# Performance work log

Measured on AMD Instinct MI355X. Metric: run time of the kernel, lower is better.

Reference implementation:

```python
import jax, jax.numpy as jnp
import numpy as np

EPS = 1e-5


def _layernorm(x, w, b):
    mu = jnp.mean(x, axis=-1, keepdims=True)
    var = jnp.var(x, axis=-1, keepdims=True)
    return (x - mu) * jax.lax.rsqrt(var + EPS) * w + b


def setup_inputs() -> dict:
    key = jax.random.key(0)
    ks = jax.random.split(key, 3)
    h, dff = 1024, 4096
    x = jax.random.normal(ks[0], (4, 2048, h), dtype=jnp.float32)
    w1 = jax.random.normal(ks[1], (h, dff), dtype=jnp.float32) * (1.0 / np.sqrt(h))
    w2 = jax.random.normal(ks[2], (dff, h), dtype=jnp.float32) * (1.0 / np.sqrt(dff))
    return {
        "x": x,
        "ln1_w": jnp.ones((h,), jnp.float32),
        "ln1_b": jnp.zeros((h,), jnp.float32),
        "ln2_w": jnp.ones((h,), jnp.float32),
        "ln2_b": jnp.zeros((h,), jnp.float32),
        "w1": w1,
        "b1": jnp.zeros((dff,), jnp.float32),
        "w2": w2,
        "b2": jnp.zeros((h,), jnp.float32),
    }


def reference(x, ln1_w, ln1_b, ln2_w, ln2_b, w1, b1, w2, b2):
    # double 1D FFT: over hidden (dim=-1) then sequence (dim=-2), keep real part
    fourier_x = jnp.fft.fft(jnp.fft.fft(x, axis=-1), axis=-2).real
    x = x + fourier_x
    x = _layernorm(x, ln1_w, ln1_b)
    # FFN: Linear -> exact GELU -> Linear (dropout is identity in eval)
    h = jax.nn.gelu(jnp.einsum("bsd,df->bsf", x, w1) + b1, approximate=False)
    x = x + jnp.einsum("bsf,fd->bsd", h, w2) + b2
    return _layernorm(x, ln2_w, ln2_b)
```

## Files before the change

### kernel.cpp

```cpp
#include <hip/hip_runtime.h>
#include <hip/hip_bf16.h>
#include <math.h>

typedef __bf16 bf16_t;
typedef __bf16 bf16x8 __attribute__((ext_vector_type(8)));
typedef __bf16 bf16x4 __attribute__((ext_vector_type(4)));
typedef float  f32x4  __attribute__((ext_vector_type(4)));

#define NROWS 8192
#define HD    1024
#define DFF   4096
#define HKEEP 513

typedef __attribute__((address_space(1))) const void* gas_cptr;
typedef __attribute__((address_space(3))) void* las_ptr;

__device__ __forceinline__ void gload_lds16(const void* g, void* l) {
  __builtin_amdgcn_global_load_lds((gas_cptr)g, (las_ptr)l, 16, 0, 0);
}

template <int N> __device__ __forceinline__ void vmw() {
  if      constexpr (N==4)  asm volatile("s_waitcnt vmcnt(4)"  ::: "memory");
  else if constexpr (N==6)  asm volatile("s_waitcnt vmcnt(6)"  ::: "memory");
  else if constexpr (N==7)  asm volatile("s_waitcnt vmcnt(7)"  ::: "memory");
  else if constexpr (N==8)  asm volatile("s_waitcnt vmcnt(8)"  ::: "memory");
  else if constexpr (N==10) asm volatile("s_waitcnt vmcnt(10)" ::: "memory");
}

__global__ __launch_bounds__(256) void transpose_to_bf16(
    const float* __restrict__ in, bf16_t* __restrict__ out, int R, int C)
{
  __shared__ float tile[32][33];
  const int bx = blockIdx.x, by = blockIdx.y;
  const int tx = threadIdx.x, ty = threadIdx.y;
  #pragma unroll
  for (int i = ty; i < 32; i += 8)
    tile[i][tx] = in[(size_t)(by*32 + i)*C + bx*32 + tx];
  __syncthreads();
  #pragma unroll
  for (int i = ty; i < 32; i += 8)
    out[(size_t)(bx*32 + i)*R + by*32 + tx] = (bf16_t)tile[tx][i];
}

#define RPB 16
#define LDW 1036
__global__ __launch_bounds__(512) void fft_h_t(
    const float* __restrict__ x, float* __restrict__ reT, float* __restrict__ imT)
{
  __shared__ float sre[RPB*LDW], sim[RPB*LDW], twc[512], tws[512];
  const int t = threadIdx.x;
  const int row0 = blockIdx.x * RPB;
  {
    float sv, cv; sincosf(-6.28318530717958647692f * (float)t * (1.0f/1024.0f), &sv, &cv);
    twc[t] = cv; tws[t] = sv;
  }
  #pragma unroll
  for (int q = 0; q < 8; ++q) {
    const int i = t + 512*q;
    const int row = i >> 8, c4 = i & 255;
    float4 v = *(const float4*)(x + (size_t)(row0+row)*HD + c4*4);
    *(float4*)&sre[row*LDW + c4*4] = v;
  }
  __syncthreads();
  const int b0i = __brev((unsigned)t) >> 22;
  const int b1i = __brev((unsigned)(t + 512)) >> 22;
  float rv[32];
  #pragma unroll
  for (int q = 0; q < 16; ++q) {
    rv[2*q]   = sre[q*LDW + b0i];
    rv[2*q+1] = sre[q*LDW + b1i];
  }
  __syncthreads();
  #pragma unroll
  for (int q = 0; q < 16; ++q) {
    sre[q*LDW + t]       = rv[2*q];
    sre[q*LDW + t + 512] = rv[2*q+1];
    sim[q*LDW + t]       = 0.0f;
    sim[q*LDW + t + 512] = 0.0f;
  }
  __syncthreads();
  for (int s = 0; s < 10; ++s) {
    const int half = 1 << s;
    const int j    = t & (half - 1);
    const int ib   = ((t >> s) << (s + 1)) | j;
    const int ti2  = j << (9 - s);
    const float wc = twc[ti2], ws = tws[ti2];
    #pragma unroll
    for (int q = 0; q < 16; ++q) {
      float* pr = &sre[q*LDW]; float* pi = &sim[q*LDW];
      const float r1 = pr[ib],      i1v = pi[ib];
      const float r2 = pr[ib+half], i2v = pi[ib+half];
      const float tr = r2*wc - i2v*ws;
      const float ti = r2*ws + i2v*wc;
      pr[ib]      = r1 + tr; pi[ib]      = i1v + ti;
      pr[ib+half] = r1 - tr; pi[ib+half] = i1v - ti;
    }
    __syncthreads();
  }
  const int tx = t & 15, th = t >> 4;
  #pragma unroll
  for (int hh = 0; hh < 17; ++hh) {
    const int h = hh*32 + th;
    if (h < HKEEP) {
      reT[(size_t)h*NROWS + row0 + tx] = sre[tx*LDW + h];
      imT[(size_t)h*NROWS + row0 + tx] = sim[tx*LDW + h];
    }
  }
}

__global__ __launch_bounds__(256) void fft_s_col(
    const float* __restrict__ reT, const float* __restrict__ imT,
    float* __restrict__ fT)
{
  __shared__ float sre[2048], sim[2048], twc[1024], tws[1024];
  const int t = threadIdx.x;
  const int h = blockIdx.x;
  const int batch = blockIdx.y;
  const size_t base = (size_t)h * NROWS + batch * 2048;
  for (int k = t; k < 1024; k += 256) {
    float sv, cv; sincosf(-6.28318530717958647692f * (float)k * (1.0f/2048.0f), &sv, &cv);
    twc[k] = cv; tws[k] = sv;
  }
  #pragma unroll
  for (int q = 0; q < 8; ++q) {
    const int i = t + 256*q;
    const int src = __brev((unsigned)i) >> 21;
    sre[i] = reT[base + src];
    sim[i] = imT[base + src];
  }
  __syncthreads();
  for (int s = 0; s < 11; ++s) {
    const int half = 1 << s;
    #pragma unroll
    for (int q = 0; q < 4; ++q) {
      const int b  = t + 256*q;
      const int j  = b & (half - 1);
      const int ib = ((b >> s) << (s + 1)) | j;
      const int ti2 = j << (10 - s);
      const float wc = twc[ti2], ws = tws[ti2];
      const float r1 = sre[ib],       i1v = sim[ib];
      const float r2 = sre[ib+half],  i2v = sim[ib+half];
      const float tr = r2*wc - i2v*ws;
      const float ti = r2*ws + i2v*wc;
      sre[ib]      = r1 + tr; sim[ib]      = i1v + ti;
      sre[ib+half] = r1 - tr; sim[ib+half] = i1v - ti;
    }
    __syncthreads();
  }
  #pragma unroll
  for (int q = 0; q < 8; ++q) {
    const int i = t + 256*q;
    fT[base + i] = sre[i];
  }
}

__global__ __launch_bounds__(256) void umadd_kernel(
    const float* __restrict__ fT, const float* __restrict__ x,
    float* __restrict__ y)
{
  __shared__ float tile[32][33];
  const int h0 = blockIdx.x * 32;
  const int b0 = blockIdx.y * 32;
  const int tx = threadIdx.x, ty = threadIdx.y;
  const int batch = b0 >> 11;
  const int s0    = b0 & 2047;
  #pragma unroll
  for (int i = ty; i < 32; i += 8) {
    const int h = h0 + i;
    float v;
    if (h <= 512) {
      v = fT[(size_t)h * NROWS + b0 + tx];
    } else {
      const int sp = (2048 - (s0 + tx)) & 2047;
      v = fT[(size_t)(1024 - h) * NROWS + (batch << 11) + sp];
    }
    tile[i][tx] = v;
  }
  __syncthreads();
  #pragma unroll
  for (int i = ty; i < 32; i += 8) {
    const size_t gi = (size_t)(b0+i)*HD + h0+tx;
    y[gi] = x[gi] + tile[tx][i];
  }
}

template <bool OUT_BF16>
__global__ __launch_bounds__(256) void layernorm_k(
    const float* __restrict__ in, const float* __restrict__ gw,
    const float* __restrict__ gb, bf16_t* __restrict__ ob, float* __restrict__ of)
{
  __shared__ float red[8];
  const size_t row = blockIdx.x;
  const int t = threadIdx.x;
  const float* xr = in + row * HD;
  float4 v = *(const float4*)(xr + t*4);
  float s = v.x + v.y + v.z + v.w;
  #pragma unroll
  for (int o = 32; o > 0; o >>= 1) s += __shfl_xor(s, o);
  if ((t & 63) == 0) red[t >> 6] = s;
  __syncthreads();
  const float mu = (red[0]+red[1]+red[2]+red[3]) * (1.0f/1024.0f);
  const float dx = v.x-mu, dy = v.y-mu, dz = v.z-mu, dw = v.w-mu;
  float sq = dx*dx + dy*dy + dz*dz + dw*dw;
  #pragma unroll
  for (int o = 32; o > 0; o >>= 1) sq += __shfl_xor(sq, o);
  if ((t & 63) == 0) red[4 + (t >> 6)] = sq;
  __syncthreads();
  const float var  = (red[4]+red[5]+red[6]+red[7]) * (1.0f/1024.0f);
  const float rstd = rsqrtf(var + 1e-5f);
  const float4 wv = *(const float4*)(gw + t*4);
  const float4 bv = *(const float4*)(gb + t*4);
  const float o0 = dx*rstd*wv.x + bv.x;
  const float o1 = dy*rstd*wv.y + bv.y;
  const float o2 = dz*rstd*wv.z + bv.z;
  const float o3 = dw*rstd*wv.w + bv.w;
  if constexpr (OUT_BF16) {
    bf16x4 o; o[0]=(bf16_t)o0; o[1]=(bf16_t)o1; o[2]=(bf16_t)o2; o[3]=(bf16_t)o3;
    *(bf16x4*)(ob + row*HD + t*4) = o;
  } else {
    float4 o; o.x=o0; o.y=o1; o.z=o2; o.w=o3;
    *(float4*)(of + row*HD + t*4) = o;
  }
}

__device__ __forceinline__ float gelu_fast(float v) {
  const float u  = 0.7978845608028654f * v * (1.0f + 0.044715f * v * v);
  const float e  = exp2f(-2.8853900817779268f * u);
  return v / (1.0f + e);
}

template <int NQ, bool GELU_OUT>
__global__ __launch_bounds__(512, 2) void gemm8r(
    const bf16_t* __restrict__ A,
    const bf16_t* __restrict__ Bt,
    const float*  __restrict__ bias,
    const bf16_t* __restrict__ resid,
    bf16_t* __restrict__ outB, float* __restrict__ outF,
    int M, int N, int K, int gx)
{
  __shared__ bf16_t As[2][2][128*64];
  __shared__ bf16_t Bs[2][2][NQ*64*64];

  const int tid  = threadIdx.x;
  const int wave = tid >> 6, lane = tid & 63;
  const int wr = wave >> 2, wc = wave & 3;
  const int lr = lane & 15, lkg = lane >> 4;

  const int nwg = gridDim.x;
  const int sid = (blockIdx.x & 7) * (nwg >> 3) + (blockIdx.x >> 3);
  const int bx = sid % gx, by = sid / gx;
  const int brow = by * 256, bcol = bx * (NQ*128);

  const int rl = lane >> 3;
  const int sg = (lane & 7) ^ rl;

  auto stageA = [&](int b, int mh, int tt) {
    #pragma unroll
    for (int l = 0; l < 2; ++l) {
      const int row = brow + l*128 + mh*64 + wave*8 + rl;
      gload_lds16(A + (size_t)row * K + tt*64 + sg*8,
                  &As[b][mh][(l*64 + wave*8)*64]);
    }
  };
  auto stageB = [&](int b, int nh, int tt) {
    #pragma unroll
    for (int l = 0; l < NQ; ++l) {
      const int rho = l*64 + wave*8 + rl;
      const int wcs = rho / (NQ*16), r = rho % (NQ*16);
      const int row = bcol + wcs*(NQ*32) + nh*(NQ*16) + r;
      gload_lds16(Bt + (size_t)row * K + tt*64 + sg*8,
                  &Bs[b][nh][(l*64 + wave*8)*64]);
    }
  };

  f32x4 acc[8][2*NQ] = {};
  bf16x8 af[4][2];
  bf16x8 bq[2][NQ][2];

  const int NT = K >> 6;
  const int NI = NT >> 1;

  stageB(0,0,0); stageA(0,0,0); stageB(0,1,0); stageA(0,1,0);
  stageB(1,0,1); stageA(1,0,1); stageB(1,1,1);
  vmw<(NQ==2 ? 6 : 4)>();
  __builtin_amdgcn_s_barrier();

  constexpr int W0 = (NQ==2) ? 10 : 8;
  constexpr int W1 = (NQ==2) ? 10 : 7;
  constexpr int W3 = (NQ==2) ? 10 : 7;
  constexpr int W4 = (NQ==2) ? 10 : 8;
  constexpr int W5 = (NQ==2) ? 10 : 7;
  constexpr int W7 = (NQ==2) ? 10 : 7;

  #define PHASE(BUF, MH, NH, DOA, DOB, STG, WN) do { \
    if constexpr (DOA) { \
      _Pragma("unroll") for (int m = 0; m < 4; ++m) \
      _Pragma("unroll") for (int ks = 0; ks < 2; ++ks) \
        af[m][ks] = *(const bf16x8*)&As[BUF][MH][(wr*64 + m*16 + lr)*64 + (((lkg + ks*4) ^ (lr & 7)) << 3)]; \
    } \
    if constexpr (DOB) { \
      _Pragma("unroll") for (int n = 0; n < NQ; ++n) \
      _Pragma("unroll") for (int ks = 0; ks < 2; ++ks) \
        bq[NH][n][ks] = *(const bf16x8*)&Bs[BUF][NH][(wc*(NQ*16) + n*16 + lr)*64 + (((lkg + ks*4) ^ (lr & 7)) << 3)]; \
    } \
    STG; \
    __builtin_amdgcn_s_barrier(); \
    asm volatile("s_waitcnt lgkmcnt(0)" ::: "memory"); \
    __builtin_amdgcn_sched_barrier(0); \
    __builtin_amdgcn_s_setprio(1); \
    _Pragma("unroll") for (int m = 0; m < 4; ++m) \
    _Pragma("unroll") for (int n = 0; n < NQ; ++n) \
    _Pragma("unroll") for (int ks = 0; ks < 2; ++ks) \
      acc[MH*4 + m][NH*NQ + n] = __builtin_amdgcn_mfma_f32_16x16x32_bf16(bq[NH][n][ks], af[m][ks], acc[MH*4 + m][NH*NQ + n], 0, 0, 0); \
    __builtin_amdgcn_s_setprio(0); \
    vmw<WN>(); \
    __builtin_amdgcn_s_barrier(); \
  } while (0)

  for (int j = 0; j < NI; ++j) {
    const int c1 = 2*j + 1;
    const int n2 = (2*j + 2 < NT) ? 2*j + 2 : NT - 1;
    const int n3 = (2*j + 3 < NT) ? 2*j + 3 : NT - 1;
    PHASE(0, 0, 0, 1, 1, stageA(1,1,c1), W0);
    PHASE(0, 0, 1, 0, 1, stageB(0,0,n2), W1);
    PHASE(0, 1, 1, 1, 0, stageA(0,0,n2), 63);
    PHASE(0, 1, 0, 0, 0, stageB(0,1,n2), W3);
    PHASE(1, 0, 0, 1, 1, stageA(0,1,n2), W4);
    PHASE(1, 0, 1, 0, 1, stageB(1,0,n3), W5);
    PHASE(1, 1, 1, 1, 0, stageA(1,0,n3), 63);
    PHASE(1, 1, 0, 0, 0, stageB(1,1,n3), W7);
  }
  #undef PHASE

  #pragma unroll
  for (int im = 0; im < 8; ++im) {
    const int row = brow + wr*128 + (im >> 2)*64 + (im & 3)*16 + lr;
    #pragma unroll
    for (int in = 0; in < 2*NQ; ++in) {
      const int col = bcol + wc*(NQ*32) + (in/NQ)*(NQ*16) + (in%NQ)*16 + lkg*4;
      const float4 bv4 = *(const float4*)(bias + col);
      float v0 = acc[im][in][0] + bv4.x;
      float v1 = acc[im][in][1] + bv4.y;
      float v2 = acc[im][in][2] + bv4.z;
      float v3 = acc[im][in][3] + bv4.w;
      if constexpr (GELU_OUT) {
        bf16x4 o;
        o[0] = (bf16_t)gelu_fast(v0); o[1] = (bf16_t)gelu_fast(v1);
        o[2] = (bf16_t)gelu_fast(v2); o[3] = (bf16_t)gelu_fast(v3);
        *(bf16x4*)(outB + (size_t)row * N + col) = o;
      } else {
        bf16x4 rr = *(const bf16x4*)(resid + (size_t)row * N + col);
        float4 o;
        o.x = v0 + (float)rr[0]; o.y = v1 + (float)rr[1];
        o.z = v2 + (float)rr[2]; o.w = v3 + (float)rr[3];
        *(float4*)(outF + (size_t)row * N + col) = o;
      }
    }
  }
}

extern "C" void kernel_launch(void* const* d_in, const int* in_sizes, int n_in,
                              void* d_out, int out_size, void* d_ws, size_t ws_size,
                              hipStream_t stream) {
  const float* x    = (const float*)d_in[0];
  const float* ln1w = (const float*)d_in[1];
  const float* ln1b = (const float*)d_in[2];
  const float* ln2w = (const float*)d_in[3];
  const float* ln2b = (const float*)d_in[4];
  const float* w1   = (const float*)d_in[5];
  const float* b1   = (const float*)d_in[6];
  const float* w2   = (const float*)d_in[7];
  const float* b2   = (const float*)d_in[8];
  float* out = (float*)d_out;

  char* ws = (char*)d_ws;
  bf16_t* w1b = (bf16_t*)(ws);
  bf16_t* w2b = (bf16_t*)(ws + (8u   << 20));
  float*  reT = (float*) (ws + (16u  << 20));
  float*  imT = (float*) (ws + (33u  << 20));
  float*  fT  = (float*) (ws + (50u  << 20));
  float*  y   = (float*) (ws + (67u  << 20));
  bf16_t* xn  = (bf16_t*)(ws + (99u  << 20));
  bf16_t* hg  = (bf16_t*)(ws + (16u  << 20));

  transpose_to_bf16<<<dim3(DFF/32, HD/32), dim3(32, 8), 0, stream>>>(w1, w1b, HD, DFF);
  transpose_to_bf16<<<dim3(HD/32, DFF/32), dim3(32, 8), 0, stream>>>(w2, w2b, DFF, HD);

  fft_h_t<<<NROWS/RPB, 512, 0, stream>>>(x, reT, imT);

  fft_s_col<<<dim3(513, 4), 256, 0, stream>>>(reT, imT, fT);

  umadd_kernel<<<dim3(HD/32, NROWS/32), dim3(32, 8), 0, stream>>>(fT, x, y);

  layernorm_k<true><<<NROWS, 256, 0, stream>>>(y, ln1w, ln1b, xn, nullptr);

  gemm8r<2, true><<<(NROWS/256)*(DFF/256), 512, 0, stream>>>(
      xn, w1b, b1, nullptr, hg, nullptr, NROWS, DFF, HD, DFF/256);
  gemm8r<1, false><<<(NROWS/256)*(HD/128), 512, 0, stream>>>(
      hg, w2b, b2, xn, nullptr, out, NROWS, HD, DFF, HD/128);

  layernorm_k<false><<<NROWS, 256, 0, stream>>>(out, ln2w, ln2b, nullptr, out);
}
```

Baseline: 311.2 us.

## Double-buffer GEMM LDS fragment registers to overlap LDS reads with MFMA

The 8-phase GEMM main loop is restructured so A and B fragment reads from LDS for the next phase are issued into alternate register sets (afX/afY, bq0X/bq0Y) while the current phase's MFMAs run. The explicit lgkmcnt(0) wait before each MFMA block is gone, and the per-phase vmcnt thresholds become a single uniform wait count. The goal is to hide LDS read latency behind matrix math. In exchange it uses more VGPRs, which could spill or strain the 2-blocks-per-CU launch bound, and it leans on the compiler to insert correct LDS waits.

New measurement: 316.9 us. About the same (+1.8%).

```diff
diff --git a/kernel.cpp b/kernel.cpp
--- a/kernel.cpp
+++ b/kernel.cpp
@@ -20,11 +20,8 @@
 }
 
 template <int N> __device__ __forceinline__ void vmw() {
-  if      constexpr (N==4)  asm volatile("s_waitcnt vmcnt(4)"  ::: "memory");
-  else if constexpr (N==6)  asm volatile("s_waitcnt vmcnt(6)"  ::: "memory");
-  else if constexpr (N==7)  asm volatile("s_waitcnt vmcnt(7)"  ::: "memory");
+  if      constexpr (N==6)  asm volatile("s_waitcnt vmcnt(6)"  ::: "memory");
   else if constexpr (N==8)  asm volatile("s_waitcnt vmcnt(8)"  ::: "memory");
-  else if constexpr (N==10) asm volatile("s_waitcnt vmcnt(10)" ::: "memory");
 }
 
 __global__ __launch_bounds__(256) void transpose_to_bf16(
@@ -230,7 +227,7 @@
 }
 
 template <int NQ, bool GELU_OUT>
-__global__ __launch_bounds__(512, 2) void gemm8r(
+__global__ __launch_bounds__(512, 2) void gemm8s(
     const bf16_t* __restrict__ A,
     const bf16_t* __restrict__ Bt,
     const float*  __restrict__ bias,
@@ -274,63 +271,63 @@
   };
 
   f32x4 acc[8][2*NQ] = {};
-  bf16x8 af[4][2];
-  bf16x8 bq[2][NQ][2];
+  bf16x8 afX[4][2], afY[4][2];
+  bf16x8 bq0X[NQ][2], bq0Y[NQ][2];
+  bf16x8 bq1[NQ][2];
 
   const int NT = K >> 6;
   const int NI = NT >> 1;
+  constexpr int WN = (NQ==2) ? 8 : 6;
+
+  #define LD_AF(DST, BUF, MH) { _Pragma("unroll") \
+    for (int m = 0; m < 4; ++m) { _Pragma("unroll") \
+    for (int ks = 0; ks < 2; ++ks) \
+      DST[m][ks] = *(const bf16x8*)&As[BUF][MH][(wr*64 + m*16 + lr)*64 + (((lkg + ks*4) ^ (lr & 7)) << 3)]; } }
+  #define LD_BQ(DST, BUF, NH) { _Pragma("unroll") \
+    for (int n = 0; n < NQ; ++n) { _Pragma("unroll") \
+    for (int ks = 0; ks < 2; ++ks) \
+      DST[n][ks] = *(const bf16x8*)&Bs[BUF][NH][(wc*(NQ*16) + n*16 + lr)*64 + (((lkg + ks*4) ^ (lr & 7)) << 3)]; } }
+  #define MM(AREG, BREG, MH, NH) do { \
+    __builtin_amdgcn_s_setprio(1); \
+    _Pragma("unroll") for (int m = 0; m < 4; ++m) { \
+    _Pragma("unroll") for (int n = 0; n < NQ; ++n) { \
+    _Pragma("unroll") for (int ks = 0; ks < 2; ++ks) \
+      acc[(MH)*4+m][(NH)*NQ+n] = __builtin_amdgcn_mfma_f32_16x16x32_bf16(BREG[n][ks], AREG[m][ks], acc[(MH)*4+m][(NH)*NQ+n], 0, 0, 0); } } \
+    __builtin_amdgcn_s_setprio(0); \
+  } while (0)
+  #define BAR() __builtin_amdgcn_s_barrier()
 
   stageB(0,0,0); stageA(0,0,0); stageB(0,1,0); stageA(0,1,0);
   stageB(1,0,1); stageA(1,0,1); stageB(1,1,1);
-  vmw<(NQ==2 ? 6 : 4)>();
-  __builtin_amdgcn_s_barrier();
-
-  constexpr int W0 = (NQ==2) ? 10 : 8;
-  constexpr int W1 = (NQ==2) ? 10 : 7;
-  constexpr int W3 = (NQ==2) ? 10 : 7;
-  constexpr int W4 = (NQ==2) ? 10 : 8;
-  constexpr int W5 = (NQ==2) ? 10 : 7;
-  constexpr int W7 = (NQ==2) ? 10 : 7;
-
-  #define PHASE(BUF, MH, NH, DOA, DOB, STG, WN) do { \
-    if constexpr (DOA) { \
-      _Pragma("unroll") for (int m = 0; m < 4; ++m) \
-      _Pragma("unroll") for (int ks = 0; ks < 2; ++ks) \
-        af[m][ks] = *(const bf16x8*)&As[BUF][MH][(wr*64 + m*16 + lr)*64 + (((lkg + ks*4) ^ (lr & 7)) << 3)]; \
-    } \
-    if constexpr (DOB) { \
-      _Pragma("unroll") for (int n = 0; n < NQ; ++n) \
-      _Pragma("unroll") for (int ks = 0; ks < 2; ++ks) \
-        bq[NH][n][ks] = *(const bf16x8*)&Bs[BUF][NH][(wc*(NQ*16) + n*16 + lr)*64 + (((lkg + ks*4) ^ (lr & 7)) << 3)]; \
-    } \
-    STG; \
-    __builtin_amdgcn_s_barrier(); \
-    asm volatile("s_waitcnt lgkmcnt(0)" ::: "memory"); \
-    __builtin_amdgcn_sched_barrier(0); \
-    __builtin_amdgcn_s_setprio(1); \
-    _Pragma("unroll") for (int m = 0; m < 4; ++m) \
-    _Pragma("unroll") for (int n = 0; n < NQ; ++n) \
-    _Pragma("unroll") for (int ks = 0; ks < 2; ++ks) \
-      acc[MH*4 + m][NH*NQ + n] = __builtin_amdgcn_mfma_f32_16x16x32_bf16(bq[NH][n][ks], af[m][ks], acc[MH*4 + m][NH*NQ + n], 0, 0, 0); \
-    __builtin_amdgcn_s_setprio(0); \
-    vmw<WN>(); \
-    __builtin_amdgcn_s_barrier(); \
-  } while (0)
+  vmw<WN>();
+  BAR();
+  LD_AF(afX, 0, 0); LD_BQ(bq0X, 0, 0);
 
   for (int j = 0; j < NI; ++j) {
     const int c1 = 2*j + 1;
     const int n2 = (2*j + 2 < NT) ? 2*j + 2 : NT - 1;
     const int n3 = (2*j + 3 < NT) ? 2*j + 3 : NT - 1;
-    PHASE(0, 0, 0, 1, 1, stageA(1,1,c1), W0);
-    PHASE(0, 0, 1, 0, 1, stageB(0,0,n2), W1);
-    PHASE(0, 1, 1, 1, 0, stageA(0,0,n2), 63);
-    PHASE(0, 1, 0, 0, 0, stageB(0,1,n2), W3);
-    PHASE(1, 0, 0, 1, 1, stageA(0,1,n2), W4);
-    PHASE(1, 0, 1, 0, 1, stageB(1,0,n3), W5);
-    PHASE(1, 1, 1, 1, 0, stageA(1,0,n3), 63);
-    PHASE(1, 1, 0, 0, 0, stageB(1,1,n3), W7);
-  }
-  #undef PHASE
+    LD_BQ(bq1, 0, 1); stageA(1,1,c1);
+    BAR(); MM(afX, bq0X, 0, 0); vmw<WN>(); BAR();
+    LD_AF(afY, 0, 1); stageB(0,0,n2);
+    BAR(); MM(afX, bq1, 0, 1); vmw<WN>(); BAR();
+    stageA(0,0,n2);
+    BAR(); MM(afY, bq1, 1, 1); vmw<WN>(); BAR();
+    LD_AF(afX, 1, 0); LD_BQ(bq0Y, 1, 0); stageB(0,1,n2);
+    BAR(); MM(afY, bq0X, 1, 0); vmw<WN>(); BAR();
+    LD_BQ(bq1, 1, 1); stageA(0,1,n2);
+    BAR(); MM(afX, bq0Y, 0, 0); vmw<WN>(); BAR();
+    LD_AF(afY, 1, 1); stageB(1,0,n3);
+    BAR(); MM(afX, bq1, 0, 1); vmw<WN>(); BAR();
+    stageA(1,0,n3);
+    BAR(); MM(afY, bq1, 1, 1); vmw<WN>(); BAR();
+    LD_AF(afX, 0, 0); LD_BQ(bq0X, 0, 0); stageB(1,1,n3);
+    BAR(); MM(afY, bq0Y, 1, 0); vmw<WN>(); BAR();
+  }
+  #undef LD_AF
+  #undef LD_BQ
+  #undef MM
+  #undef BAR
 
   #pragma unroll
   for (int im = 0; im < 8; ++im) {
@@ -394,9 +391,9 @@
 
   layernorm_k<true><<<NROWS, 256, 0, stream>>>(y, ln1w, ln1b, xn, nullptr);
 
-  gemm8r<2, true><<<(NROWS/256)*(DFF/256), 512, 0, stream>>>(
+  gemm8s<2, true><<<(NROWS/256)*(DFF/256), 512, 0, stream>>>(
       xn, w1b, b1, nullptr, hg, nullptr, NROWS, DFF, HD, DFF/256);
-  gemm8r<1, false><<<(NROWS/256)*(HD/128), 512, 0, stream>>>(
+  gemm8s<1, false><<<(NROWS/256)*(HD/128), 512, 0, stream>>>(
       hg, w2b, b2, xn, nullptr, out, NROWS, HD, DFF, HD/128);
 
   layernorm_k<false><<<NROWS, 256, 0, stream>>>(out, ln2w, ln2b, nullptr, out);
```
